# Kernel optimization log

Measured on AMD Instinct MI355X. Metric: run time of the kernel, lower is better.

The kernel has to match this reference:

```python
import jax, jax.numpy as jnp
import numpy as np

N = 50000      # nodes
E = 800000     # edges (avg degree 16)
D_IN = 128     # node_feature_dim
H = 256        # hidden_dim
EPS = 1e-5     # BatchNorm eps


def setup_inputs() -> dict:
    key = jax.random.key(0)
    ks = jax.random.split(key, 32)
    inp = {
        "x": jax.random.normal(ks[0], (N, D_IN), jnp.float32),
        "edge_index": jax.random.randint(ks[1], (2, E), 0, N, jnp.int32),
    }
    dims = [(D_IN, H), (H, H), (H, H)]
    k = 2
    for i, (din, dout) in enumerate(dims):
        s = 1.0 / np.sqrt(din)
        inp[f"Wl{i}"] = jax.random.uniform(ks[k], (din, dout), jnp.float32, -s, s); k += 1
        inp[f"bl{i}"] = jax.random.uniform(ks[k], (dout,), jnp.float32, -s, s); k += 1
        inp[f"Wr{i}"] = jax.random.uniform(ks[k], (din, dout), jnp.float32, -s, s); k += 1
        inp[f"g{i}"] = jnp.ones((dout,), jnp.float32)
        inp[f"b{i}"] = jnp.zeros((dout,), jnp.float32)
        inp[f"rm{i}"] = jax.random.normal(ks[k], (dout,), jnp.float32) * 0.1; k += 1
        inp[f"rv{i}"] = jax.random.uniform(ks[k], (dout,), jnp.float32, 0.5, 1.5); k += 1
    return inp


def _sage(x, src, dst, Wl, bl, Wr):
    # PyG SAGEConv (aggr='mean'): out = lin_l(mean_{j in N(i)} x_j) + lin_r(x_i)
    deg = jax.ops.segment_sum(jnp.ones((src.shape[0],), x.dtype), dst, num_segments=N)
    agg = jax.ops.segment_sum(x[src], dst, num_segments=N)  # [N, d_in]
    mean = agg / jnp.maximum(deg, 1.0)[:, None]
    return mean @ Wl + bl + x @ Wr


def _bn(x, g, b, rm, rv):
    # eval-mode BatchNorm1d with running stats
    return (x - rm) * (g * jax.lax.rsqrt(rv + EPS)) + b


def reference(x, edge_index,
              Wl0, bl0, Wr0, g0, b0, rm0, rv0,
              Wl1, bl1, Wr1, g1, b1, rm1, rv1,
              Wl2, bl2, Wr2, g2, b2, rm2, rv2):
    src, dst = edge_index[0], edge_index[1]
    h = jax.nn.relu(_bn(_sage(x, src, dst, Wl0, bl0, Wr0), g0, b0, rm0, rv0))
    h = jax.nn.relu(_bn(_sage(h, src, dst, Wl1, bl1, Wr1), g1, b1, rm1, rv1))
    h = _bn(_sage(h, src, dst, Wl2, bl2, Wr2), g2, b2, rm2, rv2)
    return h  # [N, H] node embeddings (dropout is identity in eval mode)
```

## Files before the change

### kernel.cpp

```cpp
#include <hip/hip_runtime.h>
#include <hip/hip_bf16.h>

#define NNODES 50000
#define NEDGES 800000
#define HID 256
#define BN_EPS 1e-5f
#define SCAN_B ((NNODES + 255) / 256)

typedef __attribute__((ext_vector_type(8))) short short8v;
typedef __attribute__((ext_vector_type(4))) float f32x4;

__device__ inline void load_lds16(const void* g, void* l) {
    __builtin_amdgcn_global_load_lds(
        (const __attribute__((address_space(1))) unsigned int*)g,
        (__attribute__((address_space(3))) unsigned int*)l, 16, 0, 0);
}

__global__ void k_zero(int* p, int n) {
    int i = blockIdx.x * blockDim.x + threadIdx.x;
    if (i < n) p[i] = 0;
}

__global__ void k_count(const int* __restrict__ ei, int* __restrict__ cnt, int nE) {
    int e = blockIdx.x * blockDim.x + threadIdx.x;
    if (e < nE) atomicAdd(&cnt[ei[nE + e]], 1);
}

__global__ void k_bsum(const int* __restrict__ cnt, int* __restrict__ loc,
                       int* __restrict__ bsum, int n) {
    __shared__ int sh[256];
    int tid = threadIdx.x;
    int i = blockIdx.x * 256 + tid;
    int v = (i < n) ? cnt[i] : 0;
    sh[tid] = v;
    __syncthreads();
    for (int off = 1; off < 256; off <<= 1) {
        int t = (tid >= off) ? sh[tid - off] : 0;
        __syncthreads();
        sh[tid] += t;
        __syncthreads();
    }
    if (i < n) loc[i] = sh[tid] - v;
    if (tid == 255) bsum[blockIdx.x] = sh[255];
}

__global__ void k_bscan(int* __restrict__ bsum, int nb) {
    __shared__ int sh[256];
    int tid = threadIdx.x;
    int v = (tid < nb) ? bsum[tid] : 0;
    sh[tid] = v;
    __syncthreads();
    for (int off = 1; off < 256; off <<= 1) {
        int t = (tid >= off) ? sh[tid - off] : 0;
        __syncthreads();
        sh[tid] += t;
        __syncthreads();
    }
    if (tid < nb) bsum[tid] = sh[tid] - v;
}

__global__ void k_addoff(const int* __restrict__ loc, const int* __restrict__ bsum,
                         int* __restrict__ rowptr, int* __restrict__ cursor,
                         int n, int nE) {
    int i = blockIdx.x * 256 + threadIdx.x;
    if (i < n) {
        int v = loc[i] + bsum[blockIdx.x];
        rowptr[i] = v;
        cursor[i] = v;
    }
    if (i == 0) rowptr[n] = nE;
}

__global__ void k_fill(const int* __restrict__ ei, int* __restrict__ cursor,
                       int* __restrict__ col, int nE) {
    int e = blockIdx.x * blockDim.x + threadIdx.x;
    if (e < nE) {
        int p = atomicAdd(&cursor[ei[nE + e]], 1);
        col[p] = ei[e];
    }
}

__global__ void k_cast(const float* __restrict__ in, __hip_bfloat16* __restrict__ out, int n) {
    int i = blockIdx.x * blockDim.x + threadIdx.x;
    int base = i * 4;
    if (base + 3 < n) {
        float4 v = *(const float4*)(in + base);
        out[base + 0] = __float2bfloat16(v.x);
        out[base + 1] = __float2bfloat16(v.y);
        out[base + 2] = __float2bfloat16(v.z);
        out[base + 3] = __float2bfloat16(v.w);
    } else {
        for (int j = base; j < n; j++) out[j] = __float2bfloat16(in[j]);
    }
}

__global__ void k_transpose6(const float* __restrict__ s0, const float* __restrict__ s1,
                             const float* __restrict__ s2, const float* __restrict__ s3,
                             const float* __restrict__ s4, const float* __restrict__ s5,
                             __hip_bfloat16* __restrict__ d0, __hip_bfloat16* __restrict__ d1,
                             __hip_bfloat16* __restrict__ d2, __hip_bfloat16* __restrict__ d3,
                             __hip_bfloat16* __restrict__ d4, __hip_bfloat16* __restrict__ d5) {
    int f = blockIdx.x * blockDim.x + threadIdx.x;
    const float* src; __hip_bfloat16* dst; int K; int i;
    if (f < 65536) {
        K = 128;
        if (f < 32768) { src = s0; dst = d0; i = f; }
        else           { src = s1; dst = d1; i = f - 32768; }
    } else {
        K = 256;
        int r = f - 65536;
        int wsel = r >> 16;
        i = r & 65535;
        src = (wsel == 0) ? s2 : (wsel == 1) ? s3 : (wsel == 2) ? s4 : s5;
        dst = (wsel == 0) ? d2 : (wsel == 1) ? d3 : (wsel == 2) ? d4 : d5;
    }
    int k = i >> 8;
    int nn = i & 255;
    dst[nn * K + k] = __float2bfloat16(src[i]);
}

template <int F>
__global__ void k_mean(const __hip_bfloat16* __restrict__ xin,
                       const int* __restrict__ rowptr, const int* __restrict__ col,
                       __hip_bfloat16* __restrict__ mean, int n) {
    int gw = (blockIdx.x * blockDim.x + threadIdx.x) >> 6;
    int lane = threadIdx.x & 63;
    if (gw >= n) return;
    int beg = rowptr[gw], end = rowptr[gw + 1];
    constexpr int D = F * 64;
    float acc[F];
#pragma unroll
    for (int j = 0; j < F; j++) acc[j] = 0.f;
    const unsigned int* base = (const unsigned int*)xin;
    int lo = (lane * F) >> 1;
    int p = beg;
    if constexpr (F == 4) {
        for (; p + 4 <= end; p += 4) {
            int s0 = col[p], s1 = col[p + 1], s2 = col[p + 2], s3 = col[p + 3];
            uint2 v0 = *(const uint2*)(base + (size_t)s0 * (D / 2) + lo);
            uint2 v1 = *(const uint2*)(base + (size_t)s1 * (D / 2) + lo);
            uint2 v2 = *(const uint2*)(base + (size_t)s2 * (D / 2) + lo);
            uint2 v3 = *(const uint2*)(base + (size_t)s3 * (D / 2) + lo);
            acc[0] += __uint_as_float(v0.x << 16) + __uint_as_float(v1.x << 16)
                    + __uint_as_float(v2.x << 16) + __uint_as_float(v3.x << 16);
            acc[1] += __uint_as_float(v0.x & 0xffff0000u) + __uint_as_float(v1.x & 0xffff0000u)
                    + __uint_as_float(v2.x & 0xffff0000u) + __uint_as_float(v3.x & 0xffff0000u);
            acc[2] += __uint_as_float(v0.y << 16) + __uint_as_float(v1.y << 16)
                    + __uint_as_float(v2.y << 16) + __uint_as_float(v3.y << 16);
            acc[3] += __uint_as_float(v0.y & 0xffff0000u) + __uint_as_float(v1.y & 0xffff0000u)
                    + __uint_as_float(v2.y & 0xffff0000u) + __uint_as_float(v3.y & 0xffff0000u);
        }
        for (; p < end; p++) {
            int s = col[p];
            uint2 v = *(const uint2*)(base + (size_t)s * (D / 2) + lo);
            acc[0] += __uint_as_float(v.x << 16);
            acc[1] += __uint_as_float(v.x & 0xffff0000u);
            acc[2] += __uint_as_float(v.y << 16);
            acc[3] += __uint_as_float(v.y & 0xffff0000u);
        }
    } else {
        for (; p + 4 <= end; p += 4) {
            int s0 = col[p], s1 = col[p + 1], s2 = col[p + 2], s3 = col[p + 3];
            unsigned int v0 = base[(size_t)s0 * (D / 2) + lo];
            unsigned int v1 = base[(size_t)s1 * (D / 2) + lo];
            unsigned int v2 = base[(size_t)s2 * (D / 2) + lo];
            unsigned int v3 = base[(size_t)s3 * (D / 2) + lo];
            acc[0] += __uint_as_float(v0 << 16) + __uint_as_float(v1 << 16)
                    + __uint_as_float(v2 << 16) + __uint_as_float(v3 << 16);
            acc[1] += __uint_as_float(v0 & 0xffff0000u) + __uint_as_float(v1 & 0xffff0000u)
                    + __uint_as_float(v2 & 0xffff0000u) + __uint_as_float(v3 & 0xffff0000u);
        }
        for (; p < end; p++) {
            unsigned int v = base[(size_t)col[p] * (D / 2) + lo];
            acc[0] += __uint_as_float(v << 16);
            acc[1] += __uint_as_float(v & 0xffff0000u);
        }
    }
    float inv = (end > beg) ? 1.f / (float)(end - beg) : 0.f;
#pragma unroll
    for (int j = 0; j < F; j++)
        mean[(size_t)gw * D + lane * F + j] = __float2bfloat16(acc[j] * inv);
}

template <int K, typename OutT, int RELU>
__launch_bounds__(256)
__global__ void k_gemm(const __hip_bfloat16* __restrict__ A1,
                       const __hip_bfloat16* __restrict__ A2,
                       const __hip_bfloat16* __restrict__ W1t,
                       const __hip_bfloat16* __restrict__ W2t,
                       const float* __restrict__ bl,
                       const float* __restrict__ g,
                       const float* __restrict__ bb,
                       const float* __restrict__ rm,
                       const float* __restrict__ rv,
                       OutT* __restrict__ out, int n) {
    __shared__ __hip_bfloat16 As[128 * 32];
    __shared__ __hip_bfloat16 Bs[128 * 32];
    int tid = threadIdx.x;
    int lane = tid & 63;
    int w = tid >> 6;
    int quad = lane >> 4;
    int ml = lane & 15;
    int rowBase = (blockIdx.x >> 1) * 128;
    int colBase = (blockIdx.x & 1) * 128;
    int wr = w >> 1, wc = w & 1;

    f32x4 acc[4][4];
#pragma unroll
    for (int i = 0; i < 4; i++)
#pragma unroll
        for (int t = 0; t < 4; t++) acc[i][t] = {0.f, 0.f, 0.f, 0.f};

    int srow = tid >> 2;
    int sbyte = (tid & 3) * 16;

    for (int s = 0; s < 2 * K; s += 32) {
        const __hip_bfloat16* A = (s < K) ? A1 : A2;
        const __hip_bfloat16* Wt = (s < K) ? W1t : W2t;
        int k0 = (s < K) ? s : (s - K);
        __syncthreads();
#pragma unroll
        for (int h = 0; h < 2; h++) {
            int r = srow + h * 64;
            int grow = rowBase + r; if (grow >= n) grow = n - 1;
            load_lds16((const char*)(A + (size_t)grow * K + k0) + sbyte,
                       (char*)As + r * 64 + sbyte);
        }
#pragma unroll
        for (int h = 0; h < 2; h++) {
            int c = srow + h * 64;
            load_lds16((const char*)(Wt + (size_t)(colBase + c) * K + k0) + sbyte,
                       (char*)Bs + c * 64 + sbyte);
        }
        __syncthreads();

        short8v af[4], bf[4];
#pragma unroll
        for (int i = 0; i < 4; i++)
            af[i] = *(const short8v*)(As + (wr * 64 + i * 16 + ml) * 32 + quad * 8);
#pragma unroll
        for (int t = 0; t < 4; t++)
            bf[t] = *(const short8v*)(Bs + (wc * 64 + t * 16 + ml) * 32 + quad * 8);
#pragma unroll
        for (int i = 0; i < 4; i++)
#pragma unroll
            for (int t = 0; t < 4; t++)
                acc[i][t] = __builtin_amdgcn_mfma_f32_16x16x32_bf16(af[i], bf[t], acc[i][t], 0, 0, 0);
    }

#pragma unroll
    for (int t = 0; t < 4; t++) {
        int c = colBase + wc * 64 + t * 16 + ml;
        float sv = g[c] * rsqrtf(rv[c] + BN_EPS);
        float tv = (bl[c] - rm[c]) * sv + bb[c];
#pragma unroll
        for (int i = 0; i < 4; i++) {
            int row0 = rowBase + wr * 64 + i * 16 + quad * 4;
#pragma unroll
            for (int r = 0; r < 4; r++) {
                int row = row0 + r;
                if (row < n) {
                    float v = acc[i][t][r] * sv + tv;
                    if (RELU) v = fmaxf(v, 0.f);
                    if constexpr (sizeof(OutT) == 2)
                        out[(size_t)row * HID + c] = (OutT)__float2bfloat16(v);
                    else
                        out[(size_t)row * HID + c] = (OutT)v;
                }
            }
        }
    }
}

extern "C" void kernel_launch(void* const* d_in, const int* in_sizes, int n_in,
                              void* d_out, int out_size, void* d_ws, size_t ws_size,
                              hipStream_t stream) {
    const float* x = (const float*)d_in[0];
    const int* ei = (const int*)d_in[1];
    const float *Wl[3], *blv[3], *Wr[3], *g[3], *bb[3], *rm[3], *rv[3];
    for (int i = 0; i < 3; i++) {
        int b = 2 + i * 7;
        Wl[i]  = (const float*)d_in[b + 0];
        blv[i] = (const float*)d_in[b + 1];
        Wr[i]  = (const float*)d_in[b + 2];
        g[i]   = (const float*)d_in[b + 3];
        bb[i]  = (const float*)d_in[b + 4];
        rm[i]  = (const float*)d_in[b + 5];
        rv[i]  = (const float*)d_in[b + 6];
    }

    char* ob = (char*)d_out;
    __hip_bfloat16* xb = (__hip_bfloat16*)ob;
    __hip_bfloat16* h0 = (__hip_bfloat16*)(ob + (size_t)NNODES * 128 * 2);

    char* w = (char*)d_ws;
    size_t off = 0;
    auto alloc = [&](size_t bytes) {
        void* p = w + off;
        off += (bytes + 255) & ~(size_t)255;
        return p;
    };
    int* rowptr = (int*)alloc((NNODES + 1) * sizeof(int));
    int* cursor = (int*)alloc(NNODES * sizeof(int));
    int* cnt    = (int*)alloc(NNODES * sizeof(int));
    int* loc    = (int*)alloc(NNODES * sizeof(int));
    int* bsum   = (int*)alloc(SCAN_B * sizeof(int));
    int* col    = (int*)alloc(NEDGES * sizeof(int));
    __hip_bfloat16* meanb = (__hip_bfloat16*)alloc((size_t)NNODES * HID * 2);
    __hip_bfloat16* h1    = (__hip_bfloat16*)alloc((size_t)NNODES * HID * 2);
    __hip_bfloat16* Wt[6];
    int Ks[6] = {128, 128, 256, 256, 256, 256};
    for (int i = 0; i < 6; i++) Wt[i] = (__hip_bfloat16*)alloc((size_t)Ks[i] * HID * 2);

    k_zero<<<SCAN_B, 256, 0, stream>>>(cnt, NNODES);
    k_count<<<(NEDGES + 255) / 256, 256, 0, stream>>>(ei, cnt, NEDGES);
    k_bsum<<<SCAN_B, 256, 0, stream>>>(cnt, loc, bsum, NNODES);
    k_bscan<<<1, 256, 0, stream>>>(bsum, SCAN_B);
    k_addoff<<<SCAN_B, 256, 0, stream>>>(loc, bsum, rowptr, cursor, NNODES, NEDGES);
    k_fill<<<(NEDGES + 255) / 256, 256, 0, stream>>>(ei, cursor, col, NEDGES);

    k_cast<<<(NNODES * 128 / 4 + 255) / 256, 256, 0, stream>>>(x, xb, NNODES * 128);

    k_transpose6<<<(327680 + 255) / 256, 256, 0, stream>>>(
        Wl[0], Wr[0], Wl[1], Wr[1], Wl[2], Wr[2],
        Wt[0], Wt[1], Wt[2], Wt[3], Wt[4], Wt[5]);

    int meanBlocks = (NNODES * 64 + 255) / 256;
    int gemmBlocks = ((NNODES + 127) / 128) * 2;

    k_mean<2><<<meanBlocks, 256, 0, stream>>>(xb, rowptr, col, meanb, NNODES);
    k_gemm<128, __hip_bfloat16, 1><<<gemmBlocks, 256, 0, stream>>>(meanb, xb, Wt[0], Wt[1],
        blv[0], g[0], bb[0], rm[0], rv[0], h0, NNODES);

    k_mean<4><<<meanBlocks, 256, 0, stream>>>(h0, rowptr, col, meanb, NNODES);
    k_gemm<256, __hip_bfloat16, 1><<<gemmBlocks, 256, 0, stream>>>(meanb, h0, Wt[2], Wt[3],
        blv[1], g[1], bb[1], rm[1], rv[1], h1, NNODES);

    k_mean<4><<<meanBlocks, 256, 0, stream>>>(h1, rowptr, col, meanb, NNODES);
    k_gemm<256, float, 0><<<gemmBlocks, 256, 0, stream>>>(meanb, h1, Wt[4], Wt[5],
        blv[2], g[2], bb[2], rm[2], rv[2], (float*)d_out, NNODES);
}
```

Before: 468.7 us.

## Widen neighbor gather to 16-byte loads and precompute CSR fill ranks

The mean-aggregation kernel now has each lane load 16 bytes (8 bf16) per neighbor. Lanes are split into sub-groups that handle different edges at once, and the partial sums are combined with cross-lane shuffles. This is meant to cut the number of memory instructions and raise memory-level parallelism in the gather. CSR construction now records each edge's rank from the counting atomic, so the fill pass needs no second atomic and no cursor array. The cost is an extra rank buffer and a shuffle reduction at the end of each row.

```diff
diff --git a/kernel.cpp b/kernel.cpp
--- a/kernel.cpp
+++ b/kernel.cpp
@@ -21,9 +21,10 @@
     if (i < n) p[i] = 0;
 }
 
-__global__ void k_count(const int* __restrict__ ei, int* __restrict__ cnt, int nE) {
+__global__ void k_countrank(const int* __restrict__ ei, int* __restrict__ cnt,
+                            int* __restrict__ rank, int nE) {
     int e = blockIdx.x * blockDim.x + threadIdx.x;
-    if (e < nE) atomicAdd(&cnt[ei[nE + e]], 1);
+    if (e < nE) rank[e] = atomicAdd(&cnt[ei[nE + e]], 1);
 }
 
 __global__ void k_bsum(const int* __restrict__ cnt, int* __restrict__ loc,
@@ -60,24 +61,16 @@
 }
 
 __global__ void k_addoff(const int* __restrict__ loc, const int* __restrict__ bsum,
-                         int* __restrict__ rowptr, int* __restrict__ cursor,
-                         int n, int nE) {
+                         int* __restrict__ rowptr, int n, int nE) {
     int i = blockIdx.x * 256 + threadIdx.x;
-    if (i < n) {
-        int v = loc[i] + bsum[blockIdx.x];
-        rowptr[i] = v;
-        cursor[i] = v;
-    }
+    if (i < n) rowptr[i] = loc[i] + bsum[blockIdx.x];
     if (i == 0) rowptr[n] = nE;
 }
 
-__global__ void k_fill(const int* __restrict__ ei, int* __restrict__ cursor,
-                       int* __restrict__ col, int nE) {
+__global__ void k_fill2(const int* __restrict__ ei, const int* __restrict__ rowptr,
+                        const int* __restrict__ rank, int* __restrict__ col, int nE) {
     int e = blockIdx.x * blockDim.x + threadIdx.x;
-    if (e < nE) {
-        int p = atomicAdd(&cursor[ei[nE + e]], 1);
-        col[p] = ei[e];
-    }
+    if (e < nE) col[rowptr[ei[nE + e]] + rank[e]] = ei[e];
 }
 
 __global__ void k_cast(const float* __restrict__ in, __hip_bfloat16* __restrict__ out, int n) {
@@ -119,67 +112,56 @@
     dst[nn * K + k] = __float2bfloat16(src[i]);
 }
 
-template <int F>
+template <int D>
 __global__ void k_mean(const __hip_bfloat16* __restrict__ xin,
                        const int* __restrict__ rowptr, const int* __restrict__ col,
                        __hip_bfloat16* __restrict__ mean, int n) {
+    constexpr int CPL = D / 8;
+    constexpr int R = 64 / CPL;
     int gw = (blockIdx.x * blockDim.x + threadIdx.x) >> 6;
     int lane = threadIdx.x & 63;
     if (gw >= n) return;
     int beg = rowptr[gw], end = rowptr[gw + 1];
-    constexpr int D = F * 64;
-    float acc[F];
-#pragma unroll
-    for (int j = 0; j < F; j++) acc[j] = 0.f;
-    const unsigned int* base = (const unsigned int*)xin;
-    int lo = (lane * F) >> 1;
-    int p = beg;
-    if constexpr (F == 4) {
-        for (; p + 4 <= end; p += 4) {
-            int s0 = col[p], s1 = col[p + 1], s2 = col[p + 2], s3 = col[p + 3];
-            uint2 v0 = *(const uint2*)(base + (size_t)s0 * (D / 2) + lo);
-            uint2 v1 = *(const uint2*)(base + (size_t)s1 * (D / 2) + lo);
-            uint2 v2 = *(const uint2*)(base + (size_t)s2 * (D / 2) + lo);
-            uint2 v3 = *(const uint2*)(base + (size_t)s3 * (D / 2) + lo);
-            acc[0] += __uint_as_float(v0.x << 16) + __uint_as_float(v1.x << 16)
-                    + __uint_as_float(v2.x << 16) + __uint_as_float(v3.x << 16);
-            acc[1] += __uint_as_float(v0.x & 0xffff0000u) + __uint_as_float(v1.x & 0xffff0000u)
-                    + __uint_as_float(v2.x & 0xffff0000u) + __uint_as_float(v3.x & 0xffff0000u);
-            acc[2] += __uint_as_float(v0.y << 16) + __uint_as_float(v1.y << 16)
-                    + __uint_as_float(v2.y << 16) + __uint_as_float(v3.y << 16);
-            acc[3] += __uint_as_float(v0.y & 0xffff0000u) + __uint_as_float(v1.y & 0xffff0000u)
-                    + __uint_as_float(v2.y & 0xffff0000u) + __uint_as_float(v3.y & 0xffff0000u);
+    int sub = lane / CPL;
+    int fpos = lane % CPL;
+    const uint4* base = (const uint4*)xin;
+
+    float acc[8];
+#pragma unroll
+    for (int j = 0; j < 8; j++) acc[j] = 0.f;
+
+    for (int p0 = beg; p0 < end; p0 += 2 * R) {
+        int p1 = p0 + sub;
+        int p2 = p0 + R + sub;
+        uint4 v1 = {0u, 0u, 0u, 0u}, v2 = {0u, 0u, 0u, 0u};
+        if (p1 < end) v1 = base[(size_t)col[p1] * CPL + fpos];
+        if (p2 < end) v2 = base[(size_t)col[p2] * CPL + fpos];
+        const unsigned int u1[4] = {v1.x, v1.y, v1.z, v1.w};
+        const unsigned int u2[4] = {v2.x, v2.y, v2.z, v2.w};
+#pragma unroll
+        for (int j = 0; j < 4; j++) {
+            acc[2 * j]     += __uint_as_float(u1[j] << 16) + __uint_as_float(u2[j] << 16);
+            acc[2 * j + 1] += __uint_as_float(u1[j] & 0xffff0000u) + __uint_as_float(u2[j] & 0xffff0000u);
         }
-        for (; p < end; p++) {
-            int s = col[p];
-            uint2 v = *(const uint2*)(base + (size_t)s * (D / 2) + lo);
-            acc[0] += __uint_as_float(v.x << 16);
-            acc[1] += __uint_as_float(v.x & 0xffff0000u);
-            acc[2] += __uint_as_float(v.y << 16);
-            acc[3] += __uint_as_float(v.y & 0xffff0000u);
-        }
-    } else {
-        for (; p + 4 <= end; p += 4) {
-            int s0 = col[p], s1 = col[p + 1], s2 = col[p + 2], s3 = col[p + 3];
-            unsigned int v0 = base[(size_t)s0 * (D / 2) + lo];
-            unsigned int v1 = base[(size_t)s1 * (D / 2) + lo];
-            unsigned int v2 = base[(size_t)s2 * (D / 2) + lo];
-            unsigned int v3 = base[(size_t)s3 * (D / 2) + lo];
-            acc[0] += __uint_as_float(v0 << 16) + __uint_as_float(v1 << 16)
-                    + __uint_as_float(v2 << 16) + __uint_as_float(v3 << 16);
-            acc[1] += __uint_as_float(v0 & 0xffff0000u) + __uint_as_float(v1 & 0xffff0000u)
-                    + __uint_as_float(v2 & 0xffff0000u) + __uint_as_float(v3 & 0xffff0000u);
-        }
-        for (; p < end; p++) {
-            unsigned int v = base[(size_t)col[p] * (D / 2) + lo];
-            acc[0] += __uint_as_float(v << 16);
-            acc[1] += __uint_as_float(v & 0xffff0000u);
-        }
-    }
-    float inv = (end > beg) ? 1.f / (float)(end - beg) : 0.f;
-#pragma unroll
-    for (int j = 0; j < F; j++)
-        mean[(size_t)gw * D + lane * F + j] = __float2bfloat16(acc[j] * inv);
+    }
+
+    if constexpr (R >= 2) {
+#pragma unroll
+        for (int j = 0; j < 8; j++) acc[j] += __shfl_xor(acc[j], 32, 64);
+    }
+    if constexpr (R == 4) {
+#pragma unroll
+        for (int j = 0; j < 8; j++) acc[j] += __shfl_xor(acc[j], 16, 64);
+    }
+
+    if (sub == 0) {
+        float inv = (end > beg) ? 1.f / (float)(end - beg) : 0.f;
+        union { uint4 v; unsigned short s[8]; } o;
+#pragma unroll
+        for (int j = 0; j < 8; j++)
+            o.s[j] = __bfloat16_as_ushort(__float2bfloat16(acc[j] * inv));
+        *(uint4*)(mean + (size_t)gw * D + fpos * 8) = o.v;
+    }
 }
 
 template <int K, typename OutT, int RELU>
@@ -301,10 +283,10 @@
         return p;
     };
     int* rowptr = (int*)alloc((NNODES + 1) * sizeof(int));
-    int* cursor = (int*)alloc(NNODES * sizeof(int));
     int* cnt    = (int*)alloc(NNODES * sizeof(int));
     int* loc    = (int*)alloc(NNODES * sizeof(int));
     int* bsum   = (int*)alloc(SCAN_B * sizeof(int));
+    int* rank   = (int*)alloc(NEDGES * sizeof(int));
     int* col    = (int*)alloc(NEDGES * sizeof(int));
     __hip_bfloat16* meanb = (__hip_bfloat16*)alloc((size_t)NNODES * HID * 2);
     __hip_bfloat16* h1    = (__hip_bfloat16*)alloc((size_t)NNODES * HID * 2);
@@ -313,11 +295,11 @@
     for (int i = 0; i < 6; i++) Wt[i] = (__hip_bfloat16*)alloc((size_t)Ks[i] * HID * 2);
 
     k_zero<<<SCAN_B, 256, 0, stream>>>(cnt, NNODES);
-    k_count<<<(NEDGES + 255) / 256, 256, 0, stream>>>(ei, cnt, NEDGES);
+    k_countrank<<<(NEDGES + 255) / 256, 256, 0, stream>>>(ei, cnt, rank, NEDGES);
     k_bsum<<<SCAN_B, 256, 0, stream>>>(cnt, loc, bsum, NNODES);
     k_bscan<<<1, 256, 0, stream>>>(bsum, SCAN_B);
-    k_addoff<<<SCAN_B, 256, 0, stream>>>(loc, bsum, rowptr, cursor, NNODES, NEDGES);
-    k_fill<<<(NEDGES + 255) / 256, 256, 0, stream>>>(ei, cursor, col, NEDGES);
+    k_addoff<<<SCAN_B, 256, 0, stream>>>(loc, bsum, rowptr, NNODES, NEDGES);
+    k_fill2<<<(NEDGES + 255) / 256, 256, 0, stream>>>(ei, rowptr, rank, col, NEDGES);
 
     k_cast<<<(NNODES * 128 / 4 + 255) / 256, 256, 0, stream>>>(x, xb, NNODES * 128);
 
@@ -328,15 +310,15 @@
     int meanBlocks = (NNODES * 64 + 255) / 256;
     int gemmBlocks = ((NNODES + 127) / 128) * 2;
 
-    k_mean<2><<<meanBlocks, 256, 0, stream>>>(xb, rowptr, col, meanb, NNODES);
+    k_mean<128><<<meanBlocks, 256, 0, stream>>>(xb, rowptr, col, meanb, NNODES);
     k_gemm<128, __hip_bfloat16, 1><<<gemmBlocks, 256, 0, stream>>>(meanb, xb, Wt[0], Wt[1],
         blv[0], g[0], bb[0], rm[0], rv[0], h0, NNODES);
 
-    k_mean<4><<<meanBlocks, 256, 0, stream>>>(h0, rowptr, col, meanb, NNODES);
+    k_mean<256><<<meanBlocks, 256, 0, stream>>>(h0, rowptr, col, meanb, NNODES);
     k_gemm<256, __hip_bfloat16, 1><<<gemmBlocks, 256, 0, stream>>>(meanb, h0, Wt[2], Wt[3],
         blv[1], g[1], bb[1], rm[1], rv[1], h1, NNODES);
 
-    k_mean<4><<<meanBlocks, 256, 0, stream>>>(h1, rowptr, col, meanb, NNODES);
+    k_mean<256><<<meanBlocks, 256, 0, stream>>>(h1, rowptr, col, meanb, NNODES);
     k_gemm<256, float, 0><<<gemmBlocks, 256, 0, stream>>>(meanb, h1, Wt[4], Wt[5],
         blv[2], g[2], bb[2], rm[2], rv[2], (float*)d_out, NNODES);
 }
```

Result: faster. 428.1 us (-8.7%).
